# Performance work log

Measured on AMD Instinct MI355X. Metric: run time of the kernel, lower is better.

The kernel has to match this reference:

```python
import jax, jax.numpy as jnp
import numpy as np

M, N, DIM = 128, 128, 256
BS = 8192
START_SIGMA = max(M, N) / 2.0
EPOCHS = 20.0
START_LR = 0.5
TAU = EPOCHS / np.log(START_SIGMA)


def setup_inputs() -> dict:
    key = jax.random.key(0)
    k_data, k_w = jax.random.split(key)
    data = jax.random.normal(k_data, (BS, DIM), dtype=jnp.float32)
    all_weights = jax.random.normal(k_w, (M, N, DIM), dtype=jnp.float32)
    return {"data": data, "all_weights": all_weights, "it": 3}


def reference(data, all_weights, it):
    m, n, dim = all_weights.shape
    bs = data.shape[0]

    # decayed sigma and learning rate (scalar schedule)
    sigma = START_SIGMA * jnp.exp(-jnp.float32(it) / jnp.float32(TAU))
    lr = START_LR * jnp.exp(-jnp.float32(it) / jnp.float32(EPOCHS))

    # pairwise Euclidean distances: [bs, m*n]
    w_flat = all_weights.reshape(m * n, dim)
    x_sq = jnp.sum(data * data, axis=1, keepdims=True)            # [bs, 1]
    w_sq = jnp.sum(w_flat * w_flat, axis=1)[None, :]              # [1, m*n]
    dists = jnp.sqrt(x_sq + w_sq - 2.0 * data @ w_flat.T)         # [bs, m*n]

    # best-matching unit grid coordinates (unravel over (m, n))
    bmu = jnp.argmin(dists, axis=1)                               # [bs]
    wins0 = (bmu // n).astype(jnp.float32)                        # row coord
    wins1 = (bmu % n).astype(jnp.float32)                         # col coord

    # Gaussian neighborhood around BMU, scaled by lr: [bs, m, n]
    d = 2.0 * sigma * sigma
    rows = jnp.arange(m, dtype=jnp.float32)
    cols = jnp.arange(n, dtype=jnp.float32)
    px = jnp.exp(-(rows[None, :] - wins0[:, None]) ** 2 / d)      # [bs, m]
    py = jnp.exp(-(cols[None, :] - wins1[:, None]) ** 2 / d)      # [bs, n]
    neighbor = (px[:, :, None] * py[:, None, :]) * lr             # [bs, m, n]

    # weighted batch update of the codebook
    denom = jnp.sum(neighbor, axis=0)[..., None]                  # [m, n, 1]
    numer = jnp.einsum('bk,bd->kd', neighbor.reshape(bs, m * n), data)
    numer = numer.reshape(m, n, dim)                              # [m, n, dim]
    new_weights = jnp.where(denom != 0, numer / denom, all_weights)
    return new_weights
```

## Files before the change

kernel.cpp:

```cpp
#include <hip/hip_runtime.h>
#include <hip/hip_fp16.h>

#define BS    8192
#define DIM   256
#define KTOT  16384
#define SLOTS 256
#define MARGIN 1.0f

typedef __attribute__((ext_vector_type(8))) _Float16 half8;
typedef __attribute__((ext_vector_type(4))) float f32x4;
typedef unsigned long long u64;

__device__ inline ushort f2h(float f) { return __half_as_ushort(__float2half(f)); }

__device__ inline void gload_lds16(const void* g, void* l) {
    __builtin_amdgcn_global_load_lds(
        (const __attribute__((address_space(1))) unsigned int*)g,
        (__attribute__((address_space(3))) unsigned int*)l, 16, 0, 0);
}

__device__ inline unsigned int fmap(float f) {
    unsigned int b = __float_as_uint(f);
    return (b & 0x80000000u) ? ~b : (b | 0x80000000u);
}
__device__ inline float unfmap(unsigned int m) {
    return (m & 0x80000000u) ? __uint_as_float(m & 0x7FFFFFFFu)
                             : __uint_as_float(~m);
}

__global__ void prep_kernel(const float* __restrict__ x, const float* __restrict__ w,
                            ushort* __restrict__ xf, ushort* __restrict__ wf,
                            float* __restrict__ wsq, float* __restrict__ S,
                            float* __restrict__ G, float* __restrict__ cntf,
                            unsigned int* __restrict__ keys, unsigned int* __restrict__ cslot,
                            const int* __restrict__ itp) {
    int idx = blockIdx.x * 256 + threadIdx.x;
    if (idx < 1048576)
        *(float4*)&S[(size_t)idx * 4] = make_float4(0.f, 0.f, 0.f, 0.f);
    if (idx < KTOT) {
        float itf = (float)itp[0];
        const float START_SIGMA = 64.0f;
        const float TAU = (float)(20.0 / 4.1588830833596715);
        float sigma = START_SIGMA * expf(-itf / TAU);
        float d2 = 2.0f * sigma * sigma;
        int i = idx >> 7, j = idx & 127;
        float diff = (float)(i - j);
        G[idx] = expf(-(diff * diff) / d2);
        cntf[idx] = 0.f;
    }
    if (idx < BS) { keys[idx] = 0xFFFFFFFFu; cslot[idx] = 0u; }

    int wid = threadIdx.x >> 6, lane = threadIdx.x & 63;
    int row = blockIdx.x * 4 + wid;
    int h = lane * 4;
    int window = h >> 5, c = (h >> 3) & 3, off = h & 7;
    if (row < BS) {
        int swpos = (window << 5) + (((c ^ ((row >> 1) & 3)) << 3)) + off;
        float4 v = *(const float4*)&x[(size_t)row * DIM + h];
        ushort4 hv;
        hv.x = f2h(v.x); hv.y = f2h(v.y); hv.z = f2h(v.z); hv.w = f2h(v.w);
        *(ushort4*)&xf[(size_t)row * DIM + swpos] = hv;
    } else {
        int r = row - BS;
        int swpos = (window << 5) + (((c ^ ((r >> 1) & 3)) << 3)) + off;
        float4 v = *(const float4*)&w[(size_t)r * DIM + h];
        ushort4 hv;
        hv.x = f2h(v.x); hv.y = f2h(v.y); hv.z = f2h(v.z); hv.w = f2h(v.w);
        *(ushort4*)&wf[(size_t)r * DIM + swpos] = hv;
        float s = v.x * v.x + v.y * v.y + v.z * v.z + v.w * v.w;
        #pragma unroll
        for (int o = 32; o; o >>= 1) s += __shfl_down(s, o, 64);
        if (lane == 0) wsq[r] = s;
    }
}

__global__ __launch_bounds__(256) void bmu_seed_kernel(
    const ushort* __restrict__ xf, const ushort* __restrict__ wf,
    const float* __restrict__ wsq, unsigned int* __restrict__ keys) {
    __shared__ ushort A[2 * 128 * 32];
    __shared__ ushort B[2 * 128 * 32];
    __shared__ float red[128][2];

    int m0 = blockIdx.x * 128;
    int k0 = blockIdx.y * 1024;
    int tid = threadIdx.x, w = tid >> 6, lane = tid & 63;
    int wm = (w & 1) * 64, wn = (w >> 1) * 64;
    int lm = lane & 15, quad = lane >> 4;
    int sw = (quad ^ ((lm >> 1) & 3)) * 8;
    int srow = lane >> 2, scol = (lane & 3) * 8;

    f32x4 acc[4][4];
    #pragma unroll
    for (int mi = 0; mi < 4; ++mi)
        #pragma unroll
        for (int ni = 0; ni < 4; ++ni)
            acc[mi][ni] = (f32x4){0.f, 0.f, 0.f, 0.f};

    for (int kb = 0; kb < DIM; kb += 64) {
        size_t axoff = (size_t)(m0 + w * 32 + srow) * DIM + kb + scol;
        size_t bxoff = (size_t)(k0 + w * 32 + srow) * DIM + kb + scol;
        gload_lds16(xf + axoff,                 &A[(w * 32) * 32]);
        gload_lds16(xf + axoff + 16 * DIM,      &A[(w * 32 + 16) * 32]);
        gload_lds16(xf + axoff + 32,            &A[4096 + (w * 32) * 32]);
        gload_lds16(xf + axoff + 16 * DIM + 32, &A[4096 + (w * 32 + 16) * 32]);
        gload_lds16(wf + bxoff,                 &B[(w * 32) * 32]);
        gload_lds16(wf + bxoff + 16 * DIM,      &B[(w * 32 + 16) * 32]);
        gload_lds16(wf + bxoff + 32,            &B[4096 + (w * 32) * 32]);
        gload_lds16(wf + bxoff + 16 * DIM + 32, &B[4096 + (w * 32 + 16) * 32]);
        __syncthreads();
        #pragma unroll 1
        for (int h = 0; h < 2; ++h) {
            const ushort* Ah = &A[h * 4096];
            const ushort* Bh = &B[h * 4096];
            half8 av[4], bv[4];
            #pragma unroll
            for (int mi = 0; mi < 4; ++mi)
                av[mi] = *(const half8*)&Ah[(wm + mi * 16 + lm) * 32 + sw];
            #pragma unroll
            for (int ni = 0; ni < 4; ++ni)
                bv[ni] = *(const half8*)&Bh[(wn + ni * 16 + lm) * 32 + sw];
            #pragma unroll
            for (int mi = 0; mi < 4; ++mi)
                #pragma unroll
                for (int ni = 0; ni < 4; ++ni)
                    acc[mi][ni] = __builtin_amdgcn_mfma_f32_16x16x32_f16(
                        av[mi], bv[ni], acc[mi][ni], 0, 0, 0);
        }
        __syncthreads();
    }
    float wsqv[4];
    #pragma unroll
    for (int ni = 0; ni < 4; ++ni) wsqv[ni] = wsq[k0 + wn + ni * 16 + lm];
    #pragma unroll
    for (int mi = 0; mi < 4; ++mi)
        #pragma unroll
        for (int r = 0; r < 4; ++r) {
            float b = 3.4e38f;
            #pragma unroll
            for (int ni = 0; ni < 4; ++ni)
                b = fminf(b, fmaf(-2.0f, acc[mi][ni][r], wsqv[ni]));
            #pragma unroll
            for (int mask = 1; mask < 16; mask <<= 1)
                b = fminf(b, __shfl_xor(b, mask, 64));
            if (lm == 0) red[wm + mi * 16 + quad * 4 + r][w >> 1] = b;
        }
    __syncthreads();
    if (tid < 128)
        atomicMin(&keys[m0 + tid], fmap(fminf(red[tid][0], red[tid][1])));
}

__global__ __launch_bounds__(256) void bmu_fused_kernel(
    const ushort* __restrict__ xf, const ushort* __restrict__ wf,
    const float* __restrict__ wsq, const unsigned int* __restrict__ keys,
    unsigned int* __restrict__ cand, unsigned int* __restrict__ cslot) {
    __shared__ ushort A[2 * 128 * 32];
    __shared__ ushort B[2 * 128 * 32];
    __shared__ float thr_l[128];

    int m0 = blockIdx.x * 128;
    int kbase = blockIdx.y * 1024;
    int tid = threadIdx.x, w = tid >> 6, lane = tid & 63;
    int wm = (w & 1) * 64, wn = (w >> 1) * 64;
    int lm = lane & 15, quad = lane >> 4;
    int sw = (quad ^ ((lm >> 1) & 3)) * 8;
    int srow = lane >> 2, scol = (lane & 3) * 8;

    if (tid < 128) thr_l[tid] = unfmap(keys[m0 + tid]) + MARGIN;
    __syncthreads();

    for (int kt = 0; kt < 8; ++kt) {
        int k0 = kbase + kt * 128;
        f32x4 acc[4][4];
        #pragma unroll
        for (int mi = 0; mi < 4; ++mi)
            #pragma unroll
            for (int ni = 0; ni < 4; ++ni)
                acc[mi][ni] = (f32x4){0.f, 0.f, 0.f, 0.f};

        for (int kb = 0; kb < DIM; kb += 64) {
            size_t axoff = (size_t)(m0 + w * 32 + srow) * DIM + kb + scol;
            size_t bxoff = (size_t)(k0 + w * 32 + srow) * DIM + kb + scol;
            gload_lds16(xf + axoff,                 &A[(w * 32) * 32]);
            gload_lds16(xf + axoff + 16 * DIM,      &A[(w * 32 + 16) * 32]);
            gload_lds16(xf + axoff + 32,            &A[4096 + (w * 32) * 32]);
            gload_lds16(xf + axoff + 16 * DIM + 32, &A[4096 + (w * 32 + 16) * 32]);
            gload_lds16(wf + bxoff,                 &B[(w * 32) * 32]);
            gload_lds16(wf + bxoff + 16 * DIM,      &B[(w * 32 + 16) * 32]);
            gload_lds16(wf + bxoff + 32,            &B[4096 + (w * 32) * 32]);
            gload_lds16(wf + bxoff + 16 * DIM + 32, &B[4096 + (w * 32 + 16) * 32]);
            __syncthreads();
            #pragma unroll 1
            for (int h = 0; h < 2; ++h) {
                const ushort* Ah = &A[h * 4096];
                const ushort* Bh = &B[h * 4096];
                half8 av[4], bv[4];
                #pragma unroll
                for (int mi = 0; mi < 4; ++mi)
                    av[mi] = *(const half8*)&Ah[(wm + mi * 16 + lm) * 32 + sw];
                #pragma unroll
                for (int ni = 0; ni < 4; ++ni)
                    bv[ni] = *(const half8*)&Bh[(wn + ni * 16 + lm) * 32 + sw];
                #pragma unroll
                for (int mi = 0; mi < 4; ++mi)
                    #pragma unroll
                    for (int ni = 0; ni < 4; ++ni)
                        acc[mi][ni] = __builtin_amdgcn_mfma_f32_16x16x32_f16(
                            av[mi], bv[ni], acc[mi][ni], 0, 0, 0);
            }
            __syncthreads();
        }
        float wsqv[4];
        #pragma unroll
        for (int ni = 0; ni < 4; ++ni) wsqv[ni] = wsq[k0 + wn + ni * 16 + lm];
        #pragma unroll
        for (int mi = 0; mi < 4; ++mi)
            #pragma unroll
            for (int r = 0; r < 4; ++r) {
                int rowi = wm + mi * 16 + quad * 4 + r;
                float thr = thr_l[rowi];
                #pragma unroll
                for (int ni = 0; ni < 4; ++ni) {
                    float sc = fmaf(-2.0f, acc[mi][ni][r], wsqv[ni]);
                    if (sc <= thr) {
                        unsigned int s = (unsigned int)(m0 + rowi);
                        unsigned int idx = atomicAdd(&cslot[s], 1u);
                        if (idx < SLOTS)
                            cand[(size_t)s * SLOTS + idx] =
                                (unsigned int)(k0 + wn + ni * 16 + lm);
                    }
                }
            }
    }
}

__global__ __launch_bounds__(256) void refine_scatter_kernel(
    const float* __restrict__ x, const float* __restrict__ w,
    const unsigned int* __restrict__ cand, const unsigned int* __restrict__ cslot,
    float* __restrict__ S, float* __restrict__ cntf) {
    int lane = threadIdx.x & 63;
    int s = blockIdx.x * 4 + (threadIdx.x >> 6);
    unsigned int n = cslot[s];
    if (n > SLOTS) n = SLOTS;
    float4 xv = *(const float4*)&x[(size_t)s * DIM + lane * 4];
    u64 best = ~0ULL;
    for (unsigned int c = 0; c < n; ++c) {
        unsigned int k = cand[(size_t)s * SLOTS + c];
        float4 wv = *(const float4*)&w[(size_t)k * DIM + lane * 4];
        float dx = xv.x - wv.x, dy = xv.y - wv.y;
        float dz = xv.z - wv.z, dw = xv.w - wv.w;
        float d = dx * dx + dy * dy + dz * dz + dw * dw;
        #pragma unroll
        for (int off = 32; off; off >>= 1) d += __shfl_xor(d, off, 64);
        u64 key = ((u64)fmap(d) << 32) | (u64)k;
        best = (key < best) ? key : best;
    }
    unsigned int k = (unsigned int)best;
    float* Sp = &S[(size_t)k * DIM + lane * 4];
    atomicAdd(Sp + 0, xv.x);
    atomicAdd(Sp + 1, xv.y);
    atomicAdd(Sp + 2, xv.z);
    atomicAdd(Sp + 3, xv.w);
    if (lane == 0) atomicAdd(&cntf[k], 1.0f);
}

__global__ __launch_bounds__(256) void gemm1_kernel(
    const float* __restrict__ G, const float* __restrict__ S, float* __restrict__ T) {
    __shared__ float Sl[128 * 68];
    int n0 = blockIdx.x * 64;
    int tid = threadIdx.x;
    #pragma unroll
    for (int q = 0; q < 8; ++q) {
        int idx = q * 256 + tid;
        int row = idx >> 4, c4 = (idx & 15) * 4;
        *(float4*)&Sl[row * 68 + c4] = *(const float4*)&S[(size_t)row * 32768 + n0 + c4];
    }
    __syncthreads();
    int ng = tid & 15, ig = tid >> 4;
    for (int pass = 0; pass < 2; ++pass) {
        int ibase = pass * 64 + ig * 4;
        float acc[4][4] = {};
        for (int a = 0; a < 128; ++a) {
            float4 sv = *(const float4*)&Sl[a * 68 + ng * 4];
            #pragma unroll
            for (int ii = 0; ii < 4; ++ii) {
                float g = G[(ibase + ii) * 128 + a];
                acc[ii][0] = fmaf(g, sv.x, acc[ii][0]);
                acc[ii][1] = fmaf(g, sv.y, acc[ii][1]);
                acc[ii][2] = fmaf(g, sv.z, acc[ii][2]);
                acc[ii][3] = fmaf(g, sv.w, acc[ii][3]);
            }
        }
        #pragma unroll
        for (int ii = 0; ii < 4; ++ii)
            *(float4*)&T[(size_t)(ibase + ii) * 32768 + n0 + ng * 4] =
                *(float4*)&acc[ii][0];
    }
}

__global__ __launch_bounds__(256) void gemm2_fin_kernel(
    const float* __restrict__ G, const float* __restrict__ T,
    const float* __restrict__ cntf, const float* __restrict__ w,
    float* __restrict__ out) {
    __shared__ float Tl[128 * 68];
    __shared__ float Pl[128];
    __shared__ float dl[128];
    int i = blockIdx.x, dq = blockIdx.y;
    int tid = threadIdx.x;
    if (tid < 128) {
        float p = 0.f;
        for (int a = 0; a < 128; ++a)
            p = fmaf(G[i * 128 + a], cntf[a * 128 + tid], p);
        Pl[tid] = p;
    }
    #pragma unroll
    for (int q = 0; q < 8; ++q) {
        int idx = q * 256 + tid;
        int row = idx >> 4, c4 = (idx & 15) * 4;
        *(float4*)&Tl[row * 68 + c4] =
            *(const float4*)&T[(size_t)i * 32768 + row * 256 + dq * 64 + c4];
    }
    __syncthreads();
    if (tid < 128) {
        float accd = 0.f;
        for (int b2 = 0; b2 < 128; ++b2)
            accd = fmaf(Pl[b2], G[b2 * 128 + tid], accd);
        dl[tid] = accd;
    }
    __syncthreads();
    int dg = tid & 15, jg = tid >> 4;
    for (int pass = 0; pass < 2; ++pass) {
        int jbase = pass * 64 + jg * 4;
        float acc[4][4] = {};
        for (int b2 = 0; b2 < 128; ++b2) {
            float4 tv = *(const float4*)&Tl[b2 * 68 + dg * 4];
            #pragma unroll
            for (int jj = 0; jj < 4; ++jj) {
                float g = G[(jbase + jj) * 128 + b2];
                acc[jj][0] = fmaf(g, tv.x, acc[jj][0]);
                acc[jj][1] = fmaf(g, tv.y, acc[jj][1]);
                acc[jj][2] = fmaf(g, tv.z, acc[jj][2]);
                acc[jj][3] = fmaf(g, tv.w, acc[jj][3]);
            }
        }
        #pragma unroll
        for (int jj = 0; jj < 4; ++jj) {
            int j = jbase + jj;
            float dv = dl[j];
            size_t e = (size_t)(i * 128 + j) * DIM + dq * 64 + dg * 4;
            float4 r;
            if (dv != 0.0f) {
                float inv = 1.0f / dv;
                r.x = acc[jj][0] * inv; r.y = acc[jj][1] * inv;
                r.z = acc[jj][2] * inv; r.w = acc[jj][3] * inv;
            } else {
                r = *(const float4*)&w[e];
            }
            *(float4*)&out[e] = r;
        }
    }
}

extern "C" void kernel_launch(void* const* d_in, const int* in_sizes, int n_in,
                              void* d_out, int out_size, void* d_ws, size_t ws_size,
                              hipStream_t stream) {
    const float* data = (const float*)d_in[0];
    const float* w    = (const float*)d_in[1];
    const int*   itp  = (const int*)d_in[2];
    float* out = (float*)d_out;

    char* ws = (char*)d_ws;
    size_t off = 0;
    float*        wsq   = (float*)(ws + off);        off += 65536;
    unsigned int* keys  = (unsigned int*)(ws + off); off += 65536;
    unsigned int* cslot = (unsigned int*)(ws + off); off += 65536;
    float*        G     = (float*)(ws + off);        off += 65536;
    float*        cntf  = (float*)(ws + off);        off += 65536;
    ushort*       xf    = (ushort*)(ws + off);       off += 4194304;
    ushort*       wf    = (ushort*)(ws + off);       off += 8388608;
    float*        S     = (float*)(ws + off);        off += 16777216;
    float*        T     = (float*)(ws + off);        off += 16777216;
    unsigned int* cand  = (unsigned int*)T;

    prep_kernel<<<(BS + KTOT) / 4, 256, 0, stream>>>(data, w, xf, wf, wsq,
                                                     S, G, cntf, keys, cslot, itp);
    bmu_seed_kernel<<<dim3(64, 16), 256, 0, stream>>>(xf, wf, wsq, keys);
    bmu_fused_kernel<<<dim3(64, 16), 256, 0, stream>>>(xf, wf, wsq, keys, cand, cslot);
    refine_scatter_kernel<<<BS / 4, 256, 0, stream>>>(data, w, cand, cslot, S, cntf);
    gemm1_kernel<<<512, 256, 0, stream>>>(G, S, T);
    gemm2_fin_kernel<<<dim3(128, 4), 256, 0, stream>>>(G, T, cntf, w, out);
}
```

Measured before the change: 333.8 us.

## Double-buffer LDS tiles to overlap global loads with MFMA in both GEMM kernels

Both the min-score kernel and the fused BMU candidate kernel now split each K-chunk into 32-wide stages across two LDS buffers. The next stage's global-to-LDS loads are issued before computing on the current buffer. In the fused kernel the loop over codebook tiles is flattened into one continuous pipeline, with the threshold/candidate epilogue run every 8 stages. This aims to hide global load latency behind MFMA work, at the cost of issuing smaller loads more often under the same number of barriers per stage.

```diff
diff --git a/kernel.cpp b/kernel.cpp
--- a/kernel.cpp
+++ b/kernel.cpp
@@ -96,37 +96,42 @@
         for (int ni = 0; ni < 4; ++ni)
             acc[mi][ni] = (f32x4){0.f, 0.f, 0.f, 0.f};
 
-    for (int kb = 0; kb < DIM; kb += 64) {
+    auto STAGE = [&](int buf, int s) {
+        int kb = s * 32;
         size_t axoff = (size_t)(m0 + w * 32 + srow) * DIM + kb + scol;
         size_t bxoff = (size_t)(k0 + w * 32 + srow) * DIM + kb + scol;
-        gload_lds16(xf + axoff,                 &A[(w * 32) * 32]);
-        gload_lds16(xf + axoff + 16 * DIM,      &A[(w * 32 + 16) * 32]);
-        gload_lds16(xf + axoff + 32,            &A[4096 + (w * 32) * 32]);
-        gload_lds16(xf + axoff + 16 * DIM + 32, &A[4096 + (w * 32 + 16) * 32]);
-        gload_lds16(wf + bxoff,                 &B[(w * 32) * 32]);
-        gload_lds16(wf + bxoff + 16 * DIM,      &B[(w * 32 + 16) * 32]);
-        gload_lds16(wf + bxoff + 32,            &B[4096 + (w * 32) * 32]);
-        gload_lds16(wf + bxoff + 16 * DIM + 32, &B[4096 + (w * 32 + 16) * 32]);
+        gload_lds16(xf + axoff,            &A[buf * 4096 + (w * 32) * 32]);
+        gload_lds16(xf + axoff + 16 * DIM, &A[buf * 4096 + (w * 32 + 16) * 32]);
+        gload_lds16(wf + bxoff,            &B[buf * 4096 + (w * 32) * 32]);
+        gload_lds16(wf + bxoff + 16 * DIM, &B[buf * 4096 + (w * 32 + 16) * 32]);
+    };
+    auto COMPUTE = [&](int buf) {
+        const ushort* Ah = &A[buf * 4096];
+        const ushort* Bh = &B[buf * 4096];
+        half8 av[4], bv[4];
+        #pragma unroll
+        for (int mi = 0; mi < 4; ++mi)
+            av[mi] = *(const half8*)&Ah[(wm + mi * 16 + lm) * 32 + sw];
+        #pragma unroll
+        for (int ni = 0; ni < 4; ++ni)
+            bv[ni] = *(const half8*)&Bh[(wn + ni * 16 + lm) * 32 + sw];
+        #pragma unroll
+        for (int mi = 0; mi < 4; ++mi)
+            #pragma unroll
+            for (int ni = 0; ni < 4; ++ni)
+                acc[mi][ni] = __builtin_amdgcn_mfma_f32_16x16x32_f16(
+                    av[mi], bv[ni], acc[mi][ni], 0, 0, 0);
+    };
+
+    STAGE(0, 0);
+    #pragma unroll 1
+    for (int it = 0; it < 4; ++it) {
         __syncthreads();
-        #pragma unroll 1
-        for (int h = 0; h < 2; ++h) {
-            const ushort* Ah = &A[h * 4096];
-            const ushort* Bh = &B[h * 4096];
-            half8 av[4], bv[4];
-            #pragma unroll
-            for (int mi = 0; mi < 4; ++mi)
-                av[mi] = *(const half8*)&Ah[(wm + mi * 16 + lm) * 32 + sw];
-            #pragma unroll
-            for (int ni = 0; ni < 4; ++ni)
-                bv[ni] = *(const half8*)&Bh[(wn + ni * 16 + lm) * 32 + sw];
-            #pragma unroll
-            for (int mi = 0; mi < 4; ++mi)
-                #pragma unroll
-                for (int ni = 0; ni < 4; ++ni)
-                    acc[mi][ni] = __builtin_amdgcn_mfma_f32_16x16x32_f16(
-                        av[mi], bv[ni], acc[mi][ni], 0, 0, 0);
-        }
+        STAGE(1, 2 * it + 1);
+        COMPUTE(0);
         __syncthreads();
+        if (it < 3) STAGE(0, 2 * it + 2);
+        COMPUTE(1);
     }
     float wsqv[4];
     #pragma unroll
@@ -166,70 +171,82 @@
     int srow = lane >> 2, scol = (lane & 3) * 8;
 
     if (tid < 128) thr_l[tid] = unfmap(keys[m0 + tid]) + MARGIN;
-    __syncthreads();
-
-    for (int kt = 0; kt < 8; ++kt) {
+
+    f32x4 acc[4][4];
+    #pragma unroll
+    for (int mi = 0; mi < 4; ++mi)
+        #pragma unroll
+        for (int ni = 0; ni < 4; ++ni)
+            acc[mi][ni] = (f32x4){0.f, 0.f, 0.f, 0.f};
+
+    auto STAGE = [&](int buf, int s) {
+        int kt = s >> 3, kb = (s & 7) * 32;
         int k0 = kbase + kt * 128;
-        f32x4 acc[4][4];
+        size_t axoff = (size_t)(m0 + w * 32 + srow) * DIM + kb + scol;
+        size_t bxoff = (size_t)(k0 + w * 32 + srow) * DIM + kb + scol;
+        gload_lds16(xf + axoff,            &A[buf * 4096 + (w * 32) * 32]);
+        gload_lds16(xf + axoff + 16 * DIM, &A[buf * 4096 + (w * 32 + 16) * 32]);
+        gload_lds16(wf + bxoff,            &B[buf * 4096 + (w * 32) * 32]);
+        gload_lds16(wf + bxoff + 16 * DIM, &B[buf * 4096 + (w * 32 + 16) * 32]);
+    };
+    auto COMPUTE = [&](int buf) {
+        const ushort* Ah = &A[buf * 4096];
+        const ushort* Bh = &B[buf * 4096];
+        half8 av[4], bv[4];
         #pragma unroll
         for (int mi = 0; mi < 4; ++mi)
+            av[mi] = *(const half8*)&Ah[(wm + mi * 16 + lm) * 32 + sw];
+        #pragma unroll
+        for (int ni = 0; ni < 4; ++ni)
+            bv[ni] = *(const half8*)&Bh[(wn + ni * 16 + lm) * 32 + sw];
+        #pragma unroll
+        for (int mi = 0; mi < 4; ++mi)
             #pragma unroll
             for (int ni = 0; ni < 4; ++ni)
-                acc[mi][ni] = (f32x4){0.f, 0.f, 0.f, 0.f};
-
-        for (int kb = 0; kb < DIM; kb += 64) {
-            size_t axoff = (size_t)(m0 + w * 32 + srow) * DIM + kb + scol;
-            size_t bxoff = (size_t)(k0 + w * 32 + srow) * DIM + kb + scol;
-            gload_lds16(xf + axoff,                 &A[(w * 32) * 32]);
-            gload_lds16(xf + axoff + 16 * DIM,      &A[(w * 32 + 16) * 32]);
-            gload_lds16(xf + axoff + 32,            &A[4096 + (w * 32) * 32]);
-            gload_lds16(xf + axoff + 16 * DIM + 32, &A[4096 + (w * 32 + 16) * 32]);
-            gload_lds16(wf + bxoff,                 &B[(w * 32) * 32]);
-            gload_lds16(wf + bxoff + 16 * DIM,      &B[(w * 32 + 16) * 32]);
-            gload_lds16(wf + bxoff + 32,            &B[4096 + (w * 32) * 32]);
-            gload_lds16(wf + bxoff + 16 * DIM + 32, &B[4096 + (w * 32 + 16) * 32]);
-            __syncthreads();
-            #pragma unroll 1
-            for (int h = 0; h < 2; ++h) {
-                const ushort* Ah = &A[h * 4096];
-                const ushort* Bh = &B[h * 4096];
-                half8 av[4], bv[4];
+                acc[mi][ni] = __builtin_amdgcn_mfma_f32_16x16x32_f16(
+                    av[mi], bv[ni], acc[mi][ni], 0, 0, 0);
+    };
+
+    STAGE(0, 0);
+    #pragma unroll 1
+    for (int it = 0; it < 32; ++it) {
+        int s0 = it * 2;
+        __syncthreads();
+        STAGE(1, s0 + 1);
+        COMPUTE(0);
+        __syncthreads();
+        if (it < 31) STAGE(0, s0 + 2);
+        COMPUTE(1);
+        if ((it & 3) == 3) {
+            int kt = (2 * it + 1) >> 3;
+            int k0 = kbase + kt * 128;
+            float wsqv[4];
+            #pragma unroll
+            for (int ni = 0; ni < 4; ++ni) wsqv[ni] = wsq[k0 + wn + ni * 16 + lm];
+            #pragma unroll
+            for (int mi = 0; mi < 4; ++mi)
                 #pragma unroll
-                for (int mi = 0; mi < 4; ++mi)
-                    av[mi] = *(const half8*)&Ah[(wm + mi * 16 + lm) * 32 + sw];
+                for (int r = 0; r < 4; ++r) {
+                    int rowi = wm + mi * 16 + quad * 4 + r;
+                    float thr = thr_l[rowi];
+                    #pragma unroll
+                    for (int ni = 0; ni < 4; ++ni) {
+                        float sc = fmaf(-2.0f, acc[mi][ni][r], wsqv[ni]);
+                        if (sc <= thr) {
+                            unsigned int s = (unsigned int)(m0 + rowi);
+                            unsigned int idx = atomicAdd(&cslot[s], 1u);
+                            if (idx < SLOTS)
+                                cand[(size_t)s * SLOTS + idx] =
+                                    (unsigned int)(k0 + wn + ni * 16 + lm);
+                        }
+                    }
+                }
+            #pragma unroll
+            for (int mi = 0; mi < 4; ++mi)
                 #pragma unroll
                 for (int ni = 0; ni < 4; ++ni)
-                    bv[ni] = *(const half8*)&Bh[(wn + ni * 16 + lm) * 32 + sw];
-                #pragma unroll
-                for (int mi = 0; mi < 4; ++mi)
-                    #pragma unroll
-                    for (int ni = 0; ni < 4; ++ni)
-                        acc[mi][ni] = __builtin_amdgcn_mfma_f32_16x16x32_f16(
-                            av[mi], bv[ni], acc[mi][ni], 0, 0, 0);
-            }
-            __syncthreads();
+                    acc[mi][ni] = (f32x4){0.f, 0.f, 0.f, 0.f};
         }
-        float wsqv[4];
-        #pragma unroll
-        for (int ni = 0; ni < 4; ++ni) wsqv[ni] = wsq[k0 + wn + ni * 16 + lm];
-        #pragma unroll
-        for (int mi = 0; mi < 4; ++mi)
-            #pragma unroll
-            for (int r = 0; r < 4; ++r) {
-                int rowi = wm + mi * 16 + quad * 4 + r;
-                float thr = thr_l[rowi];
-                #pragma unroll
-                for (int ni = 0; ni < 4; ++ni) {
-                    float sc = fmaf(-2.0f, acc[mi][ni][r], wsqv[ni]);
-                    if (sc <= thr) {
-                        unsigned int s = (unsigned int)(m0 + rowi);
-                        unsigned int idx = atomicAdd(&cslot[s], 1u);
-                        if (idx < SLOTS)
-                            cand[(size_t)s * SLOTS + idx] =
-                                (unsigned int)(k0 + wn + ni * 16 + lm);
-                    }
-                }
-            }
     }
 }
 
```

New measurement: 348.9 us. 1.05x slower.
